# Optimization experiments

Measured on AMD Instinct MI355X. Metric: run time of the kernel, lower is better.

The kernel has to match this reference:

```python
import jax, jax.numpy as jnp
import numpy as np

DIM = 1024
HEADS = 16
HEAD_DIM = DIM // HEADS
K_NEIGH = 64  # local_window, adaptive_window=False
SCALE = 1.0 / np.sqrt(HEAD_DIM)


def setup_inputs() -> dict:
    key = jax.random.key(0)
    ks = jax.random.split(key, 6)
    b, n = 1, 4096
    x = jax.random.normal(ks[0], (b, n, DIM), dtype=jnp.float32)
    cantor_coords = jax.random.uniform(ks[1], (n,), dtype=jnp.float32)
    # torch nn.Linear(dim, 3*dim): weight [3*dim, dim]; we store transposed [dim, 3*dim]
    W_qkv = jax.random.normal(ks[2], (DIM, 3 * DIM), dtype=jnp.float32) * (1.0 / np.sqrt(DIM))
    b_qkv = jax.random.normal(ks[3], (3 * DIM,), dtype=jnp.float32) * 0.01
    W_out = jax.random.normal(ks[4], (DIM, DIM), dtype=jnp.float32) * (1.0 / np.sqrt(DIM))
    b_out = jax.random.normal(ks[5], (DIM,), dtype=jnp.float32) * 0.01
    return {"x": x, "cantor_coords": cantor_coords, "W_qkv": W_qkv,
            "b_qkv": b_qkv, "W_out": W_out, "b_out": b_out}


def _routes(cantor_coords):
    # [n, n] pairwise |c_i - c_j|; k smallest -> top_k of negated distances
    d = jnp.abs(cantor_coords[:, None] - cantor_coords[None, :])
    _, idx = jax.lax.top_k(-d, K_NEIGH)  # [n, k]
    return idx


def reference(x, cantor_coords, W_qkv, b_qkv, W_out, b_out):
    b, n, _ = x.shape
    qkv = x @ W_qkv + b_qkv                          # [b, n, 3*dim]
    qkv = qkv.reshape(b, n, 3, HEADS, HEAD_DIM)
    qkv = jnp.transpose(qkv, (2, 0, 3, 1, 4))        # [3, b, h, n, d]
    q, k, v = qkv[0], qkv[1], qkv[2]

    routes = _routes(cantor_coords)                  # [n, k]
    k_g = k[:, :, routes, :]                         # [b, h, n, k, d]
    v_g = v[:, :, routes, :]
    scores = jnp.einsum('bhqd,bhqkd->bhqk', q, k_g) * SCALE
    attn = jax.nn.softmax(scores, axis=-1)           # dropout p=0 (eval)
    out = jnp.einsum('bhqk,bhqkd->bhqd', attn, v_g)  # [b, h, n, d]
    out = jnp.transpose(out, (0, 2, 1, 3)).reshape(b, n, DIM)
    return out @ W_out + b_out
```

## Files before the change

### kernel.cpp

```cpp
#include <hip/hip_runtime.h>
#include <hip/hip_bf16.h>

typedef _Float16 f16x8 __attribute__((ext_vector_type(8)));
typedef float f32x4 __attribute__((ext_vector_type(4)));
typedef unsigned long long u64;

#define NSEQ 4096
#define DIMM 1024
#define NQKV 3072

#define BAR() asm volatile("s_barrier" ::: "memory")

__device__ __forceinline__ f32x4 mfma16(f16x8 a, f16x8 b, f32x4 c) {
  return __builtin_amdgcn_mfma_f32_16x16x32_f16(a, b, c, 0, 0, 0);
}

__device__ __forceinline__ void glds16(const void* g, void* l) {
  __builtin_amdgcn_global_load_lds(
      (const __attribute__((address_space(1))) void*)g,
      (__attribute__((address_space(3))) void*)l, 16, 0, 0);
}

__global__ __launch_bounds__(256) void prep_kernel(
    const float* __restrict__ x, _Float16* __restrict__ xh,
    const float* __restrict__ Wqkv, _Float16* __restrict__ wqkvt,
    const float* __restrict__ Wout, _Float16* __restrict__ woutt,
    const float* __restrict__ cc, int* __restrict__ sorted_idx,
    float* __restrict__ csort) {
  __shared__ __align__(16) char plds[16640];
  const int bid = blockIdx.x, t = threadIdx.x;
  if (bid < 2048) {
    const int i = bid * 256 + t;
    const float4 a = ((const float4*)x)[i * 2];
    const float4 b = ((const float4*)x)[i * 2 + 1];
    f16x8 o = {(_Float16)a.x, (_Float16)a.y, (_Float16)a.z, (_Float16)a.w,
               (_Float16)b.x, (_Float16)b.y, (_Float16)b.z, (_Float16)b.w};
    ((f16x8*)xh)[i] = o;
  } else if (bid < 3072) {
    const bool qkv = bid < 2816;
    const int sub = qkv ? bid - 2048 : bid - 2816;
    const float* W = qkv ? Wqkv : Wout;
    _Float16* Wt = qkv ? wqkvt : woutt;
    const int Nn = qkv ? 3072 : 1024;
    const int k0 = (sub & 15) * 64, n0 = (sub >> 4) * 64;
    float (*tile)[65] = (float(*)[65])plds;
    const int tx = t & 63, ty = t >> 6;
    for (int rr = ty; rr < 64; rr += 4)
      tile[rr][tx] = W[(size_t)(k0 + rr) * Nn + n0 + tx];
    __syncthreads();
#pragma unroll
    for (int it = 0; it < 2; ++it) {
      const int idx = it * 256 + t;
      const int row = idx >> 3, seg = idx & 7;
      f16x8 v;
#pragma unroll
      for (int j = 0; j < 8; ++j) v[j] = (_Float16)tile[seg * 8 + j][row];
      *(f16x8*)&Wt[(size_t)(n0 + row) * 1024 + k0 + seg * 8] = v;
    }
  } else {
    float* sc = (float*)plds;
#pragma unroll
    for (int it = 0; it < 4; ++it) {
      const int i = it * 256 + t;
      ((float4*)sc)[i] = ((const float4*)cc)[i];
    }
    __syncthreads();
    const int elem = (bid - 3072) * 32 + (t >> 3);
    const int s = t & 7;
    const unsigned mybits = __float_as_uint(sc[elem]);
    int cnt = 0;
#pragma unroll 8
    for (int m = 0; m < 512; ++m) {
      const int j = s + (m << 3);
      const unsigned bj = __float_as_uint(sc[j]);
      cnt += (bj < mybits || (bj == mybits && j < elem)) ? 1 : 0;
    }
    cnt += __shfl_xor(cnt, 1);
    cnt += __shfl_xor(cnt, 2);
    cnt += __shfl_xor(cnt, 4);
    if (s == 0) {
      sorted_idx[cnt] = elem;
      csort[cnt] = sc[elem];
    }
  }
}

__global__ __launch_bounds__(512) void mask_kernel(
    const float* __restrict__ csort, const int* __restrict__ sorted_idx,
    unsigned* __restrict__ masks) {
  const int tid = threadIdx.x, lane = tid & 63, wid = tid >> 6;
  const int p = blockIdx.x * 8 + wid;
  int W0 = 64 * (p >> 6) - 64;
  W0 = min(max(W0, 0), NSEQ - 192);
  const float cp = csort[p];
  u64 key[4];
#pragma unroll
  for (int r = 0; r < 3; ++r) {
    const int w = r * 64 + lane;
    const float d = fabsf(csort[W0 + w] - cp);
    key[r] = (((u64)__float_as_uint(d)) << 20) |
             (((u64)(unsigned)sorted_idx[W0 + w]) << 8) | (unsigned)w;
  }
  key[3] = ~0ull;
#pragma unroll
  for (int k = 2; k <= 256; k <<= 1) {
#pragma unroll
    for (int j = k >> 1; j > 0; j >>= 1) {
      if (j >= 64) {
        const int rj = j >> 6;
#pragma unroll
        for (int r = 0; r < 4; ++r) {
          const int rp = r ^ rj;
          if (rp > r) {
            const bool up = (((r * 64) & k) == 0);
            const u64 a = key[r], b2 = key[rp];
            const bool sw = (a > b2) == up;
            key[r] = sw ? b2 : a;
            key[rp] = sw ? a : b2;
          }
        }
      } else {
#pragma unroll
        for (int r = 0; r < 4; ++r) {
          const u64 pv = __shfl_xor(key[r], j);
          const bool up = (((r * 64 + lane) & k) == 0);
          const bool lower = ((lane & j) == 0);
          const bool takemin = (lower == up);
          const u64 mn = key[r] < pv ? key[r] : pv;
          const u64 mx = key[r] < pv ? pv : key[r];
          key[r] = takemin ? mn : mx;
        }
      }
    }
  }
  const unsigned w0 = (unsigned)(key[0] & 0xffu);
  const unsigned hi = w0 >> 5, bit = 1u << (w0 & 31u);
  unsigned m0w = hi == 0 ? bit : 0u;
  unsigned m1w = hi == 1 ? bit : 0u;
  unsigned m2w = hi == 2 ? bit : 0u;
  unsigned m3w = hi == 3 ? bit : 0u;
  unsigned m4w = hi == 4 ? bit : 0u;
  unsigned m5w = hi == 5 ? bit : 0u;
#pragma unroll
  for (int s = 1; s < 64; s <<= 1) {
    m0w |= __shfl_xor(m0w, s);
    m1w |= __shfl_xor(m1w, s);
    m2w |= __shfl_xor(m2w, s);
    m3w |= __shfl_xor(m3w, s);
    m4w |= __shfl_xor(m4w, s);
    m5w |= __shfl_xor(m5w, s);
  }
  if (lane < 8) {
    unsigned val = 0u;
    val = lane == 0 ? m0w : val;
    val = lane == 1 ? m1w : val;
    val = lane == 2 ? m2w : val;
    val = lane == 3 ? m3w : val;
    val = lane == 4 ? m4w : val;
    val = lane == 5 ? m5w : val;
    masks[p * 8 + lane] = val;
  }
}

__device__ __forceinline__ f16x8 ldsfrag(const char* base, int r, int g) {
  return *(const f16x8*)(base + r * 128 + ((g ^ (r & 7)) << 4));
}

__device__ __forceinline__ void stage_half(const char* gbase, size_t kb, int t,
                                           char* lds_half, int tid) {
#pragma unroll
  for (int s = 0; s < 2; ++s) {
    const int rel = tid * 16 + s * 8192;
    const int r = rel >> 7;
    const int g = (rel >> 4) & 7;
    const int gg = g ^ (r & 7);
    glds16(gbase + (size_t)r * kb + t * 128 + gg * 16, lds_half + rel);
  }
}

__device__ __forceinline__ void stage_64r(const char* gbase, size_t kb, int t,
                                          char* lds8k, int tid) {
  const int rel = tid * 16;
  const int r = rel >> 7;
  const int g = (rel >> 4) & 7;
  const int gg = g ^ (r & 7);
  glds16(gbase + (size_t)r * kb + t * 128 + gg * 16, lds8k + rel);
}

__device__ __forceinline__ void rd_b3(const char* Bb, int wn, int lr, int kg,
                                      f16x8 (&bf)[3][2]) {
#pragma unroll
  for (int nt = 0; nt < 3; ++nt) {
    bf[nt][0] = ldsfrag(Bb, wn + nt * 16 + lr, kg);
    bf[nt][1] = ldsfrag(Bb, wn + nt * 16 + lr, 4 + kg);
  }
}

template <int Q>
__device__ __forceinline__ void rd_a(const char* Ab, int wm, int lr, int kg,
                                     f16x8 (&af)[2][2]) {
#pragma unroll
  for (int m = 0; m < 2; ++m) {
    af[m][0] = ldsfrag(Ab, wm + (2 * Q + m) * 16 + lr, kg);
    af[m][1] = ldsfrag(Ab, wm + (2 * Q + m) * 16 + lr, 4 + kg);
  }
}

template <int Q>
__device__ __forceinline__ void do_mfma3(const f16x8 (&af)[2][2],
                                         const f16x8 (&bf)[3][2],
                                         f32x4 (&acc)[8][3]) {
#pragma unroll
  for (int m = 0; m < 2; ++m)
#pragma unroll
    for (int nt = 0; nt < 3; ++nt) {
      acc[2 * Q + m][nt] = mfma16(af[m][0], bf[nt][0], acc[2 * Q + m][nt]);
      acc[2 * Q + m][nt] = mfma16(af[m][1], bf[nt][1], acc[2 * Q + m][nt]);
    }
}

template <bool LAST>
__device__ __forceinline__ void ktile_pair192(const char* Ag, const char* Bg,
                                              size_t kb, char* smem, int tid,
                                              int wm, int wn, int lr, int kg,
                                              int t1, int t2, int t3,
                                              f32x4 (&acc)[8][3]) {
  char* A0 = smem;
  char* A1 = smem + 32768;
  char* B0 = smem + 65536;
  char* B1 = smem + 65536 + 24576;
  f16x8 bf[3][2], af[2][2];
  rd_b3(B0, wn, lr, kg, bf);
  rd_a<0>(A0, wm, lr, kg, af);
  stage_64r(Ag, kb, t1, A1, tid);
  stage_64r(Ag + 64 * kb, kb, t1, A1 + 8192, tid);
  BAR();
  __builtin_amdgcn_s_setprio(1);
  do_mfma3<0>(af, bf, acc);
  __builtin_amdgcn_s_setprio(0);
  BAR();
  rd_a<1>(A0, wm, lr, kg, af);
  stage_64r(Ag + 128 * kb, kb, t1, A1 + 16384, tid);
  stage_64r(Ag + 192 * kb, kb, t1, A1 + 24576, tid);
  BAR();
  __builtin_amdgcn_s_setprio(1);
  do_mfma3<1>(af, bf, acc);
  __builtin_amdgcn_s_setprio(0);
  BAR();
  rd_a<2>(A0, wm, lr, kg, af);
  if (!LAST) {
    stage_64r(Bg, kb, t2, B0, tid);
    stage_64r(Bg + 64 * kb, kb, t2, B0 + 8192, tid);
  }
  BAR();
  __builtin_amdgcn_s_setprio(1);
  do_mfma3<2>(af, bf, acc);
  __builtin_amdgcn_s_setprio(0);
  BAR();
  rd_a<3>(A0, wm, lr, kg, af);
  if (!LAST) stage_64r(Bg + 128 * kb, kb, t2, B0 + 16384, tid);
  BAR();
  __builtin_amdgcn_s_setprio(1);
  do_mfma3<3>(af, bf, acc);
  __builtin_amdgcn_s_setprio(0);
  if (LAST)
    asm volatile("s_waitcnt vmcnt(0)" ::: "memory");
  else
    asm volatile("s_waitcnt vmcnt(3)" ::: "memory");
  BAR();
  rd_b3(B1, wn, lr, kg, bf);
  rd_a<0>(A1, wm, lr, kg, af);
  if (!LAST) {
    stage_64r(Ag, kb, t2, A0, tid);
    stage_64r(Ag + 64 * kb, kb, t2, A0 + 8192, tid);
  }
  BAR();
  __builtin_amdgcn_s_setprio(1);
  do_mfma3<0>(af, bf, acc);
  __builtin_amdgcn_s_setprio(0);
  BAR();
  rd_a<1>(A1, wm, lr, kg, af);
  if (!LAST) {
    stage_64r(Ag + 128 * kb, kb, t2, A0 + 16384, tid);
    stage_64r(Ag + 192 * kb, kb, t2, A0 + 24576, tid);
  }
  BAR();
  __builtin_amdgcn_s_setprio(1);
  do_mfma3<1>(af, bf, acc);
  __builtin_amdgcn_s_setprio(0);
  BAR();
  rd_a<2>(A1, wm, lr, kg, af);
  if (!LAST) {
    stage_64r(Bg, kb, t3, B1, tid);
    stage_64r(Bg + 64 * kb, kb, t3, B1 + 8192, tid);
  }
  BAR();
  __builtin_amdgcn_s_setprio(1);
  do_mfma3<2>(af, bf, acc);
  __builtin_amdgcn_s_setprio(0);
  BAR();
  rd_a<3>(A1, wm, lr, kg, af);
  if (!LAST) stage_64r(Bg + 128 * kb, kb, t3, B1 + 16384, tid);
  BAR();
  __builtin_amdgcn_s_setprio(1);
  do_mfma3<3>(af, bf, acc);
  __builtin_amdgcn_s_setprio(0);
  if (!LAST) asm volatile("s_waitcnt vmcnt(3)" ::: "memory");
  BAR();
}

__global__ __launch_bounds__(512, 2) void qkv_gemm192_kernel(
    const _Float16* __restrict__ A, const _Float16* __restrict__ Bt,
    const float* __restrict__ bias, _Float16* __restrict__ C) {
  extern __shared__ char smem[];
  const int NN = 3072;
  const size_t kb = 2048;
  const int tid = threadIdx.x;
  const int lane = tid & 63, wid = tid >> 6;
  const int lr = lane & 15, kg = lane >> 4;
  const int wm = (wid >> 2) * 128, wn = (wid & 3) * 48;
  const int bid = blockIdx.x;
  const int flat = (bid & 7) * 32 + (bid >> 3);
  const int bx = flat >> 4, by = flat & 15;
  const int m0 = bx * 256, n0 = by * 192;
  const char* Ag = (const char*)A + (size_t)m0 * kb;
  const char* Bg = (const char*)Bt + (size_t)n0 * kb;
  char* A0 = smem;
  char* B0 = smem + 65536;
  char* B1 = smem + 65536 + 24576;
  f32x4 acc[8][3] = {};
#pragma unroll
  for (int u = 0; u < 4; ++u)
    stage_64r(Ag + (size_t)(64 * u) * kb, kb, 0, A0 + u * 8192, tid);
#pragma unroll
  for (int u = 0; u < 3; ++u)
    stage_64r(Bg + (size_t)(64 * u) * kb, kb, 0, B0 + u * 8192, tid);
#pragma unroll
  for (int u = 0; u < 3; ++u)
    stage_64r(Bg + (size_t)(64 * u) * kb, kb, 1, B1 + u * 8192, tid);
  asm volatile("s_waitcnt vmcnt(3)" ::: "memory");
  BAR();
#pragma unroll 1
  for (int i = 0; i < 7; ++i)
    ktile_pair192<false>(Ag, Bg, kb, smem, tid, wm, wn, lr, kg, 2 * i + 1,
                         2 * i + 2, 2 * i + 3, acc);
  ktile_pair192<true>(Ag, Bg, kb, smem, tid, wm, wn, lr, kg, 15, 16, 17, acc);
#pragma unroll
  for (int nt = 0; nt < 3; ++nt) {
    const int col = n0 + wn + nt * 16 + lr;
    const float bv = bias[col];
#pragma unroll
    for (int mt = 0; mt < 8; ++mt) {
      const int row0 = m0 + wm + mt * 16 + kg * 4;
#pragma unroll
      for (int rr = 0; rr < 4; ++rr)
        C[(size_t)(row0 + rr) * NN + col] = (_Float16)(acc[mt][nt][rr] + bv);
    }
  }
}

__global__ __launch_bounds__(512, 2) void out_gemm128_kernel(
    const _Float16* __restrict__ A, const _Float16* __restrict__ Bt,
    const float* __restrict__ bias, float* __restrict__ C) {
  extern __shared__ char smem[];
  const size_t kb = 2048;
  const int tid = threadIdx.x;
  const int lane = tid & 63, wid = tid >> 6;
  const int lr = lane & 15, kg = lane >> 4;
  const int wm = (wid >> 2) * 64, wn = (wid & 3) * 32;
  const int bid = blockIdx.x;
  const int flat = (bid & 7) * 32 + (bid >> 3);
  const int bx = flat >> 3, by = flat & 7;
  const int m0 = bx * 128, n0 = by * 128;
  const char* Ag = (const char*)A + (size_t)m0 * kb;
  const char* Bg = (const char*)Bt + (size_t)n0 * kb;
  f32x4 acc[4][2] = {};
  stage_half(Ag, kb, 0, smem, tid);
  stage_half(Bg, kb, 0, smem + 49152, tid);
  stage_half(Ag, kb, 1, smem + 16384, tid);
  stage_half(Bg, kb, 1, smem + 49152 + 16384, tid);
  asm volatile("s_waitcnt vmcnt(4)" ::: "memory");
  BAR();
#pragma unroll
  for (int t = 0; t < 16; ++t) {
    const char* At = smem + (t % 3) * 16384;
    const char* Bb = smem + 49152 + (t % 3) * 16384;
    f16x8 bf[2][2], af[4][2];
#pragma unroll
    for (int nt = 0; nt < 2; ++nt) {
      bf[nt][0] = ldsfrag(Bb, wn + nt * 16 + lr, kg);
      bf[nt][1] = ldsfrag(Bb, wn + nt * 16 + lr, 4 + kg);
    }
#pragma unroll
    for (int m = 0; m < 4; ++m) {
      af[m][0] = ldsfrag(At, wm + m * 16 + lr, kg);
      af[m][1] = ldsfrag(At, wm + m * 16 + lr, 4 + kg);
    }
    if (t < 14) {
      stage_half(Ag, kb, t + 2, smem + ((t + 2) % 3) * 16384, tid);
      stage_half(Bg, kb, t + 2, smem + 49152 + ((t + 2) % 3) * 16384, tid);
    }
    BAR();
    __builtin_amdgcn_s_setprio(1);
#pragma unroll
    for (int m = 0; m < 4; ++m)
#pragma unroll
      for (int nt = 0; nt < 2; ++nt) {
        acc[m][nt] = mfma16(af[m][0], bf[nt][0], acc[m][nt]);
        acc[m][nt] = mfma16(af[m][1], bf[nt][1], acc[m][nt]);
      }
    __builtin_amdgcn_s_setprio(0);
    if (t < 14)
      asm volatile("s_waitcnt vmcnt(4)" ::: "memory");
    else if (t == 14)
      asm volatile("s_waitcnt vmcnt(0)" ::: "memory");
    BAR();
  }
#pragma unroll
  for (int nt = 0; nt < 2; ++nt) {
    const int col = n0 + wn + nt * 16 + lr;
    const float bv = bias[col];
#pragma unroll
    for (int mt = 0; mt < 4; ++mt) {
      const int row0 = m0 + wm + mt * 16 + kg * 4;
#pragma unroll
      for (int rr = 0; rr < 4; ++rr)
        C[(size_t)(row0 + rr) * 1024 + col] = acc[mt][nt][rr] + bv;
    }
  }
}

__global__ __launch_bounds__(256) void attn_kernel(
    const _Float16* __restrict__ qkvh, const unsigned* __restrict__ masks,
    const int* __restrict__ sorted_idx, _Float16* __restrict__ attn_h) {
  __shared__ __align__(128) char sK[24576];
  __shared__ __align__(128) char sV[24576];
  const int flat = (blockIdx.x & 7) * 128 + (blockIdx.x >> 3);
  const int b = flat & 63, h = flat >> 6;
  const int tid = threadIdx.x, lane = tid & 63, wid = tid >> 6;
  const int W0 = min(max(64 * b - 64, 0), NSEQ - 192);
  const int lrow16 = lane & 15, kgrp = lane >> 4;
  int ridx[6];
#pragma unroll
  for (int c = 0; c < 6; ++c)
    ridx[c] = sorted_idx[W0 + c * 32 + wid * 8 + (lane >> 3)];
#pragma unroll
  for (int c = 0; c < 6; ++c) {
    const int o = c * 4096 + wid * 1024 + lane * 16;
    const int row = o >> 7;
    const int inrow = (o & 127) ^ ((row & 7) << 4);
    glds16((const char*)qkvh + (size_t)ridx[c] * 6144 + 2048 + h * 128 + inrow,
           sK + o);
  }
  f16x8 vreg[6];
#pragma unroll
  for (int c = 0; c < 6; ++c) {
    const int o = c * 4096 + wid * 1024 + lane * 16;
    vreg[c] = *(const f16x8*)((const char*)qkvh + (size_t)ridx[c] * 6144 +
                              4096 + h * 128 + (o & 127));
  }
  const int p_base = b * 64 + wid * 16;
  const int orig_q = sorted_idx[p_base + lrow16];
  const char* qp = (const char*)qkvh + (size_t)orig_q * 6144 + h * 128 + kgrp * 16;
  const f16x8 aq0 = *(const f16x8*)qp;
  const f16x8 aq1 = *(const f16x8*)(qp + 64);
  unsigned mb[4];
#pragma unroll
  for (int r = 0; r < 4; ++r) {
    const int p = p_base + kgrp * 4 + r;
    const uint4 wa = *(const uint4*)&masks[p * 8];
    const uint2 wb2 = *(const uint2*)&masks[p * 8 + 4];
    const unsigned wsv6[6] = {wa.x, wa.y, wa.z, wa.w, wb2.x, wb2.y};
    unsigned bits = 0;
#pragma unroll
    for (int n = 0; n < 12; ++n)
      bits |= ((wsv6[n >> 1] >> (((n & 1) << 4) + lrow16)) & 1u) << n;
    mb[r] = bits;
  }
  const int lrot = lane & 7;
#pragma unroll
  for (int c = 0; c < 6; ++c) {
    const int o = c * 4096 + wid * 1024 + lane * 16;
    const int k = o >> 7;
    const int d0 = (o & 127) >> 1;
#pragma unroll
    for (int ee = 0; ee < 8; ++ee) {
      const int e = (ee + lrot) & 7;
      const int d = d0 + e;
      *(_Float16*)(sV + d * 384 + ((2 * k) ^ ((d & 7) << 4))) = vreg[c][e];
    }
  }
  __syncthreads();
  float sv[12][4];
#pragma unroll
  for (int n = 0; n < 12; ++n) {
    const int j = n * 16 + lrow16;
    const int sw = (j & 7) << 4;
    const char* kr = sK + j * 128;
    const f16x8 b0 = *(const f16x8*)(kr + ((kgrp * 16) ^ sw));
    const f16x8 b1 = *(const f16x8*)(kr + ((64 + kgrp * 16) ^ sw));
    f32x4 a = {};
    a = mfma16(aq0, b0, a);
    a = mfma16(aq1, b1, a);
#pragma unroll
    for (int r = 0; r < 4; ++r)
      sv[n][r] = ((mb[r] >> n) & 1u) ? a[r] * 0.125f : -1e30f;
  }
#pragma unroll
  for (int r = 0; r < 4; ++r) {
    float m = sv[0][r];
#pragma unroll
    for (int n = 1; n < 12; ++n) m = fmaxf(m, sv[n][r]);
    m = fmaxf(m, __shfl_xor(m, 1));
    m = fmaxf(m, __shfl_xor(m, 2));
    m = fmaxf(m, __shfl_xor(m, 4));
    m = fmaxf(m, __shfl_xor(m, 8));
    float s = 0.f;
#pragma unroll
    for (int n = 0; n < 12; ++n) {
      const float e = __expf(sv[n][r] - m);
      sv[n][r] = e;
      s += e;
    }
    s += __shfl_xor(s, 1);
    s += __shfl_xor(s, 2);
    s += __shfl_xor(s, 4);
    s += __shfl_xor(s, 8);
    const float rinv = 1.f / s;
#pragma unroll
    for (int n = 0; n < 12; ++n) sv[n][r] *= rinv;
  }
  __syncthreads();
#pragma unroll
  for (int n = 0; n < 12; ++n) {
#pragma unroll
    for (int r = 0; r < 4; ++r) {
      const int lrw = wid * 16 + kgrp * 4 + r;
      const int cb = (n * 16 + lrow16) * 2;
      *(_Float16*)(sK + lrw * 384 + (cb ^ ((lrw & 7) << 4))) = (_Float16)sv[n][r];
    }
  }
  __syncthreads();
  f32x4 oacc[4] = {};
  const int arow = wid * 16 + lrow16;
  const int swa = (arow & 7) << 4;
#pragma unroll
  for (int kt = 0; kt < 6; ++kt) {
    const int kbo = kt * 64 + kgrp * 16;
    const f16x8 pa = *(const f16x8*)(sK + arow * 384 + (kbo ^ swa));
#pragma unroll
    for (int nt = 0; nt < 4; ++nt) {
      const int d = nt * 16 + lrow16;
      const f16x8 vb = *(const f16x8*)(sV + d * 384 + (kbo ^ ((d & 7) << 4)));
      oacc[nt] = mfma16(pa, vb, oacc[nt]);
    }
  }
#pragma unroll
  for (int r = 0; r < 4; ++r) {
    const int p = p_base + kgrp * 4 + r;
    const int orig = sorted_idx[p];
    _Float16* op = attn_h + (size_t)orig * DIMM + h * 64;
#pragma unroll
    for (int nt = 0; nt < 4; ++nt)
      op[nt * 16 + lrow16] = (_Float16)oacc[nt][r];
  }
}

extern "C" void kernel_launch(void* const* d_in, const int* in_sizes, int n_in,
                              void* d_out, int out_size, void* d_ws, size_t ws_size,
                              hipStream_t stream) {
  const float* x = (const float*)d_in[0];
  const float* cc = (const float*)d_in[1];
  const float* Wqkv = (const float*)d_in[2];
  const float* bqkv = (const float*)d_in[3];
  const float* Wout = (const float*)d_in[4];
  const float* bout = (const float*)d_in[5];
  char* ws = (char*)d_ws;

  _Float16* xh = (_Float16*)(ws + 0);
  _Float16* wqkvt = (_Float16*)(ws + 8388608);
  _Float16* woutt = (_Float16*)(ws + 14680064);
  _Float16* qkvh = (_Float16*)(ws + 16777216);
  _Float16* atnh = (_Float16*)(ws + 41943040);
  int* sidx = (int*)(ws + 50331648);
  float* csort = (float*)(ws + 50348032);
  unsigned* msk = (unsigned*)(ws + 50364416);

  hipFuncSetAttribute((const void*)qkv_gemm192_kernel,
                      hipFuncAttributeMaxDynamicSharedMemorySize, 114688);
  hipFuncSetAttribute((const void*)out_gemm128_kernel,
                      hipFuncAttributeMaxDynamicSharedMemorySize, 98304);

  prep_kernel<<<3200, 256, 0, stream>>>(x, xh, Wqkv, wqkvt, Wout, woutt, cc,
                                        sidx, csort);
  mask_kernel<<<512, 512, 0, stream>>>(csort, sidx, msk);
  qkv_gemm192_kernel<<<256, 512, 114688, stream>>>(xh, wqkvt, bqkv, qkvh);
  attn_kernel<<<1024, 256, 0, stream>>>(qkvh, msk, sidx, atnh);
  out_gemm128_kernel<<<256, 512, 98304, stream>>>(atnh, woutt, bout,
                                                  (float*)d_out);
}
```

Before: 102.2 us.

## Scatter QKV rows into sorted order in GEMM epilogue and remap block tiles

The prep kernel now also records each element's rank in the sorted coordinate order. The QKV GEMM epilogue uses that rank to write each output row at its sorted position. Attention can then read K/V windows and Q rows contiguously, without gathering through sorted_idx. The block-to-tile mapping of both GEMMs is also changed to group tiles per XCD differently for L2 reuse. The cost is scattered row stores in the GEMM epilogue and an extra rank read.

```diff
diff --git a/kernel.cpp b/kernel.cpp
--- a/kernel.cpp
+++ b/kernel.cpp
@@ -26,7 +26,7 @@
     const float* __restrict__ Wqkv, _Float16* __restrict__ wqkvt,
     const float* __restrict__ Wout, _Float16* __restrict__ woutt,
     const float* __restrict__ cc, int* __restrict__ sorted_idx,
-    float* __restrict__ csort) {
+    float* __restrict__ csort, int* __restrict__ ranko) {
   __shared__ __align__(16) char plds[16640];
   const int bid = blockIdx.x, t = threadIdx.x;
   if (bid < 2048) {
@@ -81,6 +81,7 @@
     if (s == 0) {
       sorted_idx[cnt] = elem;
       csort[cnt] = sc[elem];
+      ranko[elem] = cnt;
     }
   }
 }
@@ -311,7 +312,8 @@
 
 __global__ __launch_bounds__(512, 2) void qkv_gemm192_kernel(
     const _Float16* __restrict__ A, const _Float16* __restrict__ Bt,
-    const float* __restrict__ bias, _Float16* __restrict__ C) {
+    const float* __restrict__ bias, const int* __restrict__ ranko,
+    _Float16* __restrict__ C) {
   extern __shared__ char smem[];
   const int NN = 3072;
   const size_t kb = 2048;
@@ -319,9 +321,9 @@
   const int lane = tid & 63, wid = tid >> 6;
   const int lr = lane & 15, kg = lane >> 4;
   const int wm = (wid >> 2) * 128, wn = (wid & 3) * 48;
-  const int bid = blockIdx.x;
-  const int flat = (bid & 7) * 32 + (bid >> 3);
-  const int bx = flat >> 4, by = flat & 15;
+  const int r8 = blockIdx.x & 7, idx = blockIdx.x >> 3;
+  const int bx = (r8 & 3) * 4 + (idx >> 3);
+  const int by = (r8 >> 2) * 8 + (idx & 7);
   const int m0 = bx * 256, n0 = by * 192;
   const char* Ag = (const char*)A + (size_t)m0 * kb;
   const char* Bg = (const char*)Bt + (size_t)n0 * kb;
@@ -346,15 +348,18 @@
                          2 * i + 2, 2 * i + 3, acc);
   ktile_pair192<true>(Ag, Bg, kb, smem, tid, wm, wn, lr, kg, 15, 16, 17, acc);
 #pragma unroll
-  for (int nt = 0; nt < 3; ++nt) {
-    const int col = n0 + wn + nt * 16 + lr;
-    const float bv = bias[col];
-#pragma unroll
-    for (int mt = 0; mt < 8; ++mt) {
-      const int row0 = m0 + wm + mt * 16 + kg * 4;
+  for (int mt = 0; mt < 8; ++mt) {
+    const int row0 = m0 + wm + mt * 16 + kg * 4;
+    int srow[4];
+#pragma unroll
+    for (int rr = 0; rr < 4; ++rr) srow[rr] = ranko[row0 + rr];
+#pragma unroll
+    for (int nt = 0; nt < 3; ++nt) {
+      const int col = n0 + wn + nt * 16 + lr;
+      const float bv = bias[col];
 #pragma unroll
       for (int rr = 0; rr < 4; ++rr)
-        C[(size_t)(row0 + rr) * NN + col] = (_Float16)(acc[mt][nt][rr] + bv);
+        C[(size_t)srow[rr] * NN + col] = (_Float16)(acc[mt][nt][rr] + bv);
     }
   }
 }
@@ -368,9 +373,9 @@
   const int lane = tid & 63, wid = tid >> 6;
   const int lr = lane & 15, kg = lane >> 4;
   const int wm = (wid >> 2) * 64, wn = (wid & 3) * 32;
-  const int bid = blockIdx.x;
-  const int flat = (bid & 7) * 32 + (bid >> 3);
-  const int bx = flat >> 3, by = flat & 7;
+  const int r8 = blockIdx.x & 7, idx = blockIdx.x >> 3;
+  const int bx = (r8 & 3) * 8 + (idx >> 2);
+  const int by = (r8 >> 2) * 4 + (idx & 3);
   const int m0 = bx * 128, n0 = by * 128;
   const char* Ag = (const char*)A + (size_t)m0 * kb;
   const char* Bg = (const char*)Bt + (size_t)n0 * kb;
@@ -431,7 +436,7 @@
 }
 
 __global__ __launch_bounds__(256) void attn_kernel(
-    const _Float16* __restrict__ qkvh, const unsigned* __restrict__ masks,
+    const _Float16* __restrict__ qkvs, const unsigned* __restrict__ masks,
     const int* __restrict__ sorted_idx, _Float16* __restrict__ attn_h) {
   __shared__ __align__(128) char sK[24576];
   __shared__ __align__(128) char sV[24576];
@@ -440,28 +445,24 @@
   const int tid = threadIdx.x, lane = tid & 63, wid = tid >> 6;
   const int W0 = min(max(64 * b - 64, 0), NSEQ - 192);
   const int lrow16 = lane & 15, kgrp = lane >> 4;
-  int ridx[6];
-#pragma unroll
-  for (int c = 0; c < 6; ++c)
-    ridx[c] = sorted_idx[W0 + c * 32 + wid * 8 + (lane >> 3)];
 #pragma unroll
   for (int c = 0; c < 6; ++c) {
     const int o = c * 4096 + wid * 1024 + lane * 16;
     const int row = o >> 7;
     const int inrow = (o & 127) ^ ((row & 7) << 4);
-    glds16((const char*)qkvh + (size_t)ridx[c] * 6144 + 2048 + h * 128 + inrow,
+    glds16((const char*)qkvs + (size_t)(W0 + row) * 6144 + 2048 + h * 128 + inrow,
            sK + o);
   }
   f16x8 vreg[6];
 #pragma unroll
   for (int c = 0; c < 6; ++c) {
     const int o = c * 4096 + wid * 1024 + lane * 16;
-    vreg[c] = *(const f16x8*)((const char*)qkvh + (size_t)ridx[c] * 6144 +
+    vreg[c] = *(const f16x8*)((const char*)qkvs + (size_t)(W0 + (o >> 7)) * 6144 +
                               4096 + h * 128 + (o & 127));
   }
   const int p_base = b * 64 + wid * 16;
-  const int orig_q = sorted_idx[p_base + lrow16];
-  const char* qp = (const char*)qkvh + (size_t)orig_q * 6144 + h * 128 + kgrp * 16;
+  const char* qp =
+      (const char*)qkvs + (size_t)(p_base + lrow16) * 6144 + h * 128 + kgrp * 16;
   const f16x8 aq0 = *(const f16x8*)qp;
   const f16x8 aq1 = *(const f16x8*)(qp + 64);
   unsigned mb[4];
@@ -580,11 +581,12 @@
   _Float16* xh = (_Float16*)(ws + 0);
   _Float16* wqkvt = (_Float16*)(ws + 8388608);
   _Float16* woutt = (_Float16*)(ws + 14680064);
-  _Float16* qkvh = (_Float16*)(ws + 16777216);
+  _Float16* qkvs = (_Float16*)(ws + 16777216);
   _Float16* atnh = (_Float16*)(ws + 41943040);
   int* sidx = (int*)(ws + 50331648);
   float* csort = (float*)(ws + 50348032);
-  unsigned* msk = (unsigned*)(ws + 50364416);
+  int* rankb = (int*)(ws + 50364416);
+  unsigned* msk = (unsigned*)(ws + 50380800);
 
   hipFuncSetAttribute((const void*)qkv_gemm192_kernel,
                       hipFuncAttributeMaxDynamicSharedMemorySize, 114688);
@@ -592,10 +594,11 @@
                       hipFuncAttributeMaxDynamicSharedMemorySize, 98304);
 
   prep_kernel<<<3200, 256, 0, stream>>>(x, xh, Wqkv, wqkvt, Wout, woutt, cc,
-                                        sidx, csort);
+                                        sidx, csort, rankb);
   mask_kernel<<<512, 512, 0, stream>>>(csort, sidx, msk);
-  qkv_gemm192_kernel<<<256, 512, 114688, stream>>>(xh, wqkvt, bqkv, qkvh);
-  attn_kernel<<<1024, 256, 0, stream>>>(qkvh, msk, sidx, atnh);
+  qkv_gemm192_kernel<<<256, 512, 114688, stream>>>(xh, wqkvt, bqkv, rankb,
+                                                   qkvs);
+  attn_kernel<<<1024, 256, 0, stream>>>(qkvs, msk, sidx, atnh);
   out_gemm128_kernel<<<256, 512, 98304, stream>>>(atnh, woutt, bout,
                                                   (float*)d_out);
 }
```

Result: no change. 102.8 us (+0.6%).
